# Kernel tuning notes

Hardware: AMD Instinct MI355X
Metric: run time of the kernel (lower is better)

Reference implementation:

```python
import jax, jax.numpy as jnp
from jax import lax
import numpy as np

NF = 64      # feature channels
G = 8        # deformable groups
K = 3        # kernel size
KK = K * K
NLEVEL = 3

PARAM_SHAPES = {
    "c0a_w": (64, 3, 3, 3), "c0a_b": (64,),
    "c0r_w1": (64, 64, 3, 3), "c0r_b1": (64,), "c0r_w2": (64, 64, 3, 3), "c0r_b2": (64,),
    "c0b_w": (64, 64, 3, 3), "c0b_b": (64,),
    "d_r1w1": (64, 64, 3, 3), "d_r1b1": (64,), "d_r1w2": (64, 64, 3, 3), "d_r1b2": (64,),
    "d_r2w1": (64, 64, 3, 3), "d_r2b1": (64,), "d_r2w2": (64, 64, 3, 3), "d_r2b2": (64,),
    "d_cw": (64, 64, 3, 3), "d_cb": (64,),
    "off_c1w": (64, 128, 3, 3), "off_c1b": (64,),
    "off_rw1": (64, 64, 3, 3), "off_rb1": (64,), "off_rw2": (64, 64, 3, 3), "off_rb2": (64,),
    "off_c2w": (64, 64, 3, 3), "off_c2b": (64,),
    "mrg_c1w": (64, 128, 3, 3), "mrg_c1b": (64,),
    "mrg_rw1": (64, 64, 3, 3), "mrg_rb1": (64,), "mrg_rw2": (64, 64, 3, 3), "mrg_rb2": (64,),
    "mrg_c2w": (64, 64, 3, 3), "mrg_c2b": (64,),
    "dcn_om_w": (216, 64, 3, 3), "dcn_om_b": (216,),
    "dcn_w": (64, 64, 3, 3), "dcn_b": (64,),
}


def setup_inputs() -> dict:
    key = jax.random.key(0)
    inp = {"images": jax.random.normal(key, (2, 3, 3, 160, 160), jnp.float32)}
    for i, (name, sh) in enumerate(PARAM_SHAPES.items()):
        if len(sh) == 1:
            inp[name] = jnp.zeros(sh, jnp.float32)
        else:
            inp[name] = jax.random.normal(jax.random.fold_in(key, i + 1), sh, jnp.float32) * 0.05
    return inp


def conv(x, w, b):
    y = lax.conv_general_dilated(x, w, (1, 1), 'SAME',
                                 dimension_numbers=('NCHW', 'OIHW', 'NCHW'))
    return y + b[None, :, None, None]


def lrelu(x):  # nn.LeakyReLU default slope 0.01
    return jnp.where(x >= 0, x, 0.01 * x)


def resblock(x, w1, b1, w2, b2):
    return x + conv(jax.nn.relu(conv(x, w1, b1)), w2, b2)


def maxpool3s2(x):  # MaxPool2d(3, 2, 1)
    return lax.reduce_window(x, -jnp.inf, lax.max, (1, 1, 3, 3), (1, 1, 2, 2),
                             ((0, 0), (0, 0), (1, 1), (1, 1)))


def offnet(x, c1w, c1b, rw1, rb1, rw2, rb2, c2w, c2b):
    # Conv-LReLU, then the SAME residual block applied twice (shared), Conv-LReLU
    x = lrelu(conv(x, c1w, c1b))
    x = resblock(x, rw1, rb1, rw2, rb2)
    x = resblock(x, rw1, rb1, rw2, rb2)
    return lrelu(conv(x, c2w, c2b))


def dcn(x, feat, om_w, om_b, w, b):
    # Modulated deformable conv v2 (extra_offset_mask=True): offsets/mask from feat.
    B, C, H, W = x.shape
    Cg = C // G
    om = conv(feat, om_w, om_b)                       # [B, 3*G*KK, H, W]
    o1, o2, m = jnp.split(om, 3, axis=1)
    dy = o1.reshape(B, G, KK, H, W)
    dx = o2.reshape(B, G, KK, H, W)
    mask = jax.nn.sigmoid(m).reshape(B, G, KK, H, W)
    ky, kx = jnp.meshgrid(jnp.arange(K, dtype=x.dtype) - 1,
                          jnp.arange(K, dtype=x.dtype) - 1, indexing='ij')
    py = dy + jnp.arange(H, dtype=x.dtype)[:, None] + ky.reshape(KK)[:, None, None]
    px = dx + jnp.arange(W, dtype=x.dtype) + kx.reshape(KK)[:, None, None]
    y0 = jnp.floor(py); x0 = jnp.floor(px)
    wy = py - y0; wx = px - x0
    y0i = y0.astype(jnp.int32); x0i = x0.astype(jnp.int32)
    xg = x.reshape(B, G, Cg, H * W)

    def gather(yi, xi, wt):
        valid = (yi >= 0) & (yi < H) & (xi >= 0) & (xi < W)
        idx = jnp.clip(yi, 0, H - 1) * W + jnp.clip(xi, 0, W - 1)      # [B,G,KK,H,W]
        g = jnp.take_along_axis(
            xg, jnp.broadcast_to(idx.reshape(B, G, 1, KK * H * W), (B, G, Cg, KK * H * W)),
            axis=3).reshape(B, G, Cg, KK, H, W)
        return g * (wt * valid)[:, :, None]

    val = (gather(y0i, x0i, (1 - wy) * (1 - wx))
           + gather(y0i, x0i + 1, (1 - wy) * wx)
           + gather(y0i + 1, x0i, wy * (1 - wx))
           + gather(y0i + 1, x0i + 1, wy * wx))
    val = val * mask[:, :, None]                      # [B,G,Cg,KK,H,W]
    wr = w.reshape(w.shape[0], G, Cg, KK)
    return jnp.einsum('bgckhw,ogck->bohw', val, wr) + b[None, :, None, None]


def reference(images, c0a_w, c0a_b, c0r_w1, c0r_b1, c0r_w2, c0r_b2, c0b_w, c0b_b,
              d_r1w1, d_r1b1, d_r1w2, d_r1b2, d_r2w1, d_r2b1, d_r2w2, d_r2b2, d_cw, d_cb,
              off_c1w, off_c1b, off_rw1, off_rb1, off_rw2, off_rb2, off_c2w, off_c2b,
              mrg_c1w, mrg_c1b, mrg_rw1, mrg_rb1, mrg_rw2, mrg_rb2, mrg_c2w, mrg_c2b,
              dcn_om_w, dcn_om_b, dcn_w, dcn_b):
    b, n, c, h, w = images.shape
    x = images.reshape(b * n, c, h, w)
    x = conv(x, c0a_w, c0a_b)
    x = resblock(x, c0r_w1, c0r_b1, c0r_w2, c0r_b2)
    feat = lrelu(conv(x, c0b_w, c0b_b))
    pyrs = [feat]
    for _ in range(NLEVEL - 1):  # downs share one parameter set ([module]*n)
        y = resblock(pyrs[-1], d_r1w1, d_r1b1, d_r1w2, d_r1b2)
        y = resblock(y, d_r2w1, d_r2b1, d_r2w2, d_r2b2)
        y = lrelu(maxpool3s2(conv(y, d_cw, d_cb)))
        pyrs.append(y)
    laps = [p.reshape(b, n, NF, p.shape[-2], p.shape[-1]) for p in pyrs]
    offp = (off_c1w, off_c1b, off_rw1, off_rb1, off_rw2, off_rb2, off_c2w, off_c2b)
    mrgp = (mrg_c1w, mrg_c1b, mrg_rw1, mrg_rb1, mrg_rw2, mrg_rb2, mrg_c2w, mrg_c2b)
    cv = n // 2
    for view in range(n):  # sequential in-place update (center view mutates mid-loop)
        po = offnet(jnp.concatenate([laps[-1][:, cv], laps[-1][:, view]], 1), *offp)
        laps[-1] = laps[-1].at[:, view].set(
            dcn(laps[-1][:, view], po, dcn_om_w, dcn_om_b, dcn_w, dcn_b))
        for level in range(NLEVEL - 2, -1, -1):
            cf = laps[level][:, cv]
            lf = laps[level][:, view]
            off = offnet(jnp.concatenate([cf, lf], 1), *offp)
            B_, C_, H_, W_ = po.shape
            po_up = jax.image.resize(po, (B_, C_, H_ * 2, W_ * 2), 'bilinear')
            off = offnet(jnp.concatenate([off, po_up * 2.0], 1), *mrgp)
            laps[level] = laps[level].at[:, view].set(
                dcn(lf, off, dcn_om_w, dcn_om_b, dcn_w, dcn_b))
            po = off
    return tuple(laps)
```

## Files before the change

kernel.cpp:

```cpp
#include <hip/hip_runtime.h>
#include <math.h>

using short8 = __attribute__((ext_vector_type(8))) short;
using f32x4  = __attribute__((ext_vector_type(4))) float;

struct Tab8 { long o[8]; };

__device__ __forceinline__ unsigned short f2bf(float f) {
    unsigned u = __builtin_bit_cast(unsigned, f);
    unsigned r = u + 0x7FFFu + ((u >> 16) & 1u);
    return (unsigned short)(r >> 16);
}
__device__ __forceinline__ float bf2f(unsigned short h) {
    unsigned u = ((unsigned)h) << 16;
    return __builtin_bit_cast(float, u);
}

struct WDesc { const float* w; int Ci, O, Opad; long off; };
struct WDescs { WDesc d[18]; };

__global__ __launch_bounds__(256) void prep_w_k(WDescs ds, unsigned short* wp)
{
    const WDesc d = ds.d[blockIdx.y];
    const int ncib = (d.Ci + 15) >> 4;
    const int n = ncib * d.Opad * 288;
    const int idx = blockIdx.x * 256 + threadIdx.x;
    if (idx >= n) return;
    const int within = idx % 288;
    const int o = (idx / 288) % d.Opad;
    const int cib = idx / (288 * d.Opad);
    const int t = within >> 5, q = within & 31;
    const int ci = (cib << 4) + (q & 15);
    float v = 0.0f;
    if (o < d.O && ci < d.Ci) v = d.w[((long)o * d.Ci + ci) * 9 + t];
    const unsigned short hi = f2bf(v);
    const unsigned short lo = f2bf(v - bf2f(hi));
    wp[d.off + idx] = (q < 16) ? hi : lo;
}

__global__ __launch_bounds__(256) void prep_dcnw_k(const float* __restrict__ w,
                                                   unsigned short* __restrict__ out)
{
    const int idx = blockIdx.x * 256 + threadIdx.x;
    if (idx >= 36 * 64 * 32) return;
    const int q = idx & 31, o = (idx >> 5) & 63, kb = idx >> 11;
    const float v = w[o * 576 + kb * 16 + (q & 15)];
    const unsigned short hi = f2bf(v);
    out[idx] = (q < 16) ? hi : f2bf(v - bf2f(hi));
}

__global__ __launch_bounds__(256, 2) void conv_mfma_k(
    const float* __restrict__ in1, Tab8 t1, int cin1,
    const float* __restrict__ in2, Tab8 t2, int cin2,
    const unsigned short* __restrict__ wp,
    const float* __restrict__ bias,
    const float* __restrict__ res, Tab8 trr, int hasres,
    float* __restrict__ out, Tab8 to,
    int O, int H, int W, int act)
{
    __shared__ unsigned short in_t[12960];
    __shared__ unsigned short w_t[18944];
    const int tid = threadIdx.x;
    const int b = blockIdx.z;
    const int Opad = gridDim.y << 6;
    const int cobase = blockIdx.y << 6;
    const int tilesX = (W + 15) >> 4;
    const int tx = blockIdx.x % tilesX, ty = blockIdx.x / tilesX;
    const int x0 = tx << 4, y0 = ty << 4;
    const int HW = H * W;
    const int cin_tot = cin1 + cin2;
    const int ncib = (cin_tot + 15) >> 4;
    const int wv = tid >> 6, lane = tid & 63;
    const int lxx = lane & 15, kb = lane >> 4;
    const long o1 = t1.o[b], o2 = t2.o[b];

    f32x4 acc[4][4];
    #pragma unroll
    for (int i = 0; i < 4; ++i)
        #pragma unroll
        for (int j = 0; j < 4; ++j)
            acc[i][j] = (f32x4){0.f, 0.f, 0.f, 0.f};

    for (int cib = 0; cib < ncib; ++cib) {
        __syncthreads();
        const unsigned short* slab = wp + ((long)cib * Opad + cobase) * 288;
        #pragma unroll
        for (int i = 0; i < 9; ++i) {
            const int c = tid + (i << 8);
            const int row = c / 36, col = c - row * 36;
            *(short8*)&w_t[row * 296 + (col << 3)] =
                *(const short8*)(slab + row * 288 + (col << 3));
        }
        if (tid < 144) {
            const int yy = tid >> 3, rp = tid & 7;
            const int g = (cib << 4) + (rp << 1);
            const float* s0 = nullptr;
            const float* s1 = nullptr;
            if (g < cin_tot)
                s0 = (g < cin1) ? in1 + o1 + (long)g * HW
                                : in2 + o2 + (long)(g - cin1) * HW;
            if (g + 1 < cin_tot)
                s1 = (g + 1 < cin1) ? in1 + o1 + (long)(g + 1) * HW
                                    : in2 + o2 + (long)(g + 1 - cin1) * HW;
            const int gy = y0 - 1 + yy;
            const bool yok = (gy >= 0) && (gy < H);
            #pragma unroll
            for (int xx = 0; xx < 18; ++xx) {
                const int gx = x0 - 1 + xx;
                const bool ok = yok && (gx >= 0) && (gx < W);
                const float v0 = (ok && s0) ? s0[gy * W + gx] : 0.0f;
                const float v1 = (ok && s1) ? s1[gy * W + gx] : 0.0f;
                const unsigned short h0 = f2bf(v0), h1 = f2bf(v1);
                const unsigned short l0 = f2bf(v0 - bf2f(h0));
                const unsigned short l1 = f2bf(v1 - bf2f(h1));
                unsigned short* base = &in_t[(yy * 18 + xx) * 40];
                *(unsigned*)(base + (rp << 1))      = (unsigned)h0 | ((unsigned)h1 << 16);
                *(unsigned*)(base + 16 + (rp << 1)) = (unsigned)l0 | ((unsigned)l1 << 16);
            }
        }
        __syncthreads();
        #pragma unroll
        for (int ky = 0; ky < 3; ++ky) {
            #pragma unroll
            for (int kx = 0; kx < 3; ++kx) {
                const int tap = ky * 3 + kx;
                short8 a[4], b1[4], b2[4];
                #pragma unroll
                for (int mt = 0; mt < 4; ++mt)
                    a[mt] = *(const short8*)&w_t[(mt * 16 + lxx) * 296 + tap * 32 + kb * 8];
                #pragma unroll
                for (int rr = 0; rr < 4; ++rr) {
                    const int pbase = ((wv * 4 + rr + ky) * 18 + lxx + kx) * 40;
                    b1[rr] = *(const short8*)&in_t[pbase + kb * 8];
                    b2[rr] = *(const short8*)&in_t[pbase + (kb ^ 2) * 8];
                }
                #pragma unroll
                for (int mt = 0; mt < 4; ++mt)
                    #pragma unroll
                    for (int rr = 0; rr < 4; ++rr) {
                        acc[mt][rr] = __builtin_amdgcn_mfma_f32_16x16x32_bf16(
                            a[mt], b1[rr], acc[mt][rr], 0, 0, 0);
                        acc[mt][rr] = __builtin_amdgcn_mfma_f32_16x16x32_bf16(
                            a[mt], b2[rr], acc[mt][rr], 0, 0, 0);
                    }
            }
        }
    }

    const int x = x0 + lxx;
    const bool xok = (x < W);
    const long ob = to.o[b], rb = trr.o[b];
    #pragma unroll
    for (int mt = 0; mt < 4; ++mt) {
        const int col0 = cobase + mt * 16 + kb * 4;
        float bvv[4];
        #pragma unroll
        for (int j = 0; j < 4; ++j)
            bvv[j] = (col0 + j < O) ? bias[col0 + j] : 0.0f;
        #pragma unroll
        for (int rr = 0; rr < 4; ++rr) {
            const int y = y0 + wv * 4 + rr;
            if (y >= H) continue;
            #pragma unroll
            for (int j = 0; j < 4; ++j) {
                const int coj = col0 + j;
                if (coj >= O || !xok) continue;
                float v = acc[mt][rr][j] + bvv[j];
                if (hasres) v += res[rb + (long)coj * HW + (long)y * W + x];
                if (act == 1) v = fmaxf(v, 0.0f);
                else if (act == 2) v = (v >= 0.0f) ? v : 0.01f * v;
                out[ob + (long)coj * HW + (long)y * W + x] = v;
            }
        }
    }
}

__global__ __launch_bounds__(256) void pool_lrelu_k(
    const float* __restrict__ in, float* __restrict__ out, int H, int W)
{
    const int Ho = H / 2, Wo = W / 2;
    const int n = blockIdx.y;
    const int i = blockIdx.x * 256 + threadIdx.x;
    if (i >= Ho * Wo) return;
    const int ho = i / Wo, wo = i % Wo;
    const float* p = in + (long)n * H * W;
    float m = -1e30f;
    #pragma unroll
    for (int dy = 0; dy < 3; ++dy) {
        const int y = 2 * ho - 1 + dy;
        if (y < 0 || y >= H) continue;
        #pragma unroll
        for (int dx = 0; dx < 3; ++dx) {
            const int x = 2 * wo - 1 + dx;
            if (x < 0 || x >= W) continue;
            m = fmaxf(m, p[y * W + x]);
        }
    }
    out[(long)n * Ho * Wo + i] = (m >= 0.0f) ? m : 0.01f * m;
}

__global__ __launch_bounds__(256) void resize2x_k(
    const float* __restrict__ in, float* __restrict__ out, int H, int W)
{
    const int Ho = 2 * H, Wo = 2 * W;
    const int n = blockIdx.y;
    const int i = blockIdx.x * 256 + threadIdx.x;
    if (i >= Ho * Wo) return;
    const int ho = i / Wo, wo = i % Wo;
    float cy = fminf(fmaxf(0.5f * (ho + 0.5f) - 0.5f, 0.0f), (float)(H - 1));
    float cx = fminf(fmaxf(0.5f * (wo + 0.5f) - 0.5f, 0.0f), (float)(W - 1));
    const int y0 = (int)cy, x0 = (int)cx;
    const int y1 = min(y0 + 1, H - 1), x1 = min(x0 + 1, W - 1);
    const float fy = cy - y0, fx = cx - x0;
    const float* p = in + (long)n * H * W;
    const float v = (1.0f - fy) * ((1.0f - fx) * p[y0 * W + x0] + fx * p[y0 * W + x1])
                  + fy * ((1.0f - fx) * p[y1 * W + x0] + fx * p[y1 * W + x1]);
    out[(long)n * Ho * Wo + i] = 2.0f * v;
}

__global__ __launch_bounds__(256) void nhwc_k(
    const float* __restrict__ src, Tab8 ts, float* __restrict__ dst,
    long dstride, int HW)
{
    __shared__ float t[64][65];
    const int tid = threadIdx.x;
    const int vb = blockIdx.y;
    const int pos0 = blockIdx.x * 64;
    const float* s = src + ts.o[vb];
    float* d = dst + (long)vb * dstride;
    const int l = tid & 63, q = tid >> 6;
    #pragma unroll
    for (int i = 0; i < 16; ++i) {
        const int c = q * 16 + i;
        t[c][l] = s[(long)c * HW + pos0 + l];
    }
    __syncthreads();
    #pragma unroll
    for (int i = 0; i < 16; ++i) {
        const int p = q * 16 + i;
        d[(long)(pos0 + p) * 64 + l] = t[l][p];
    }
}

__global__ __launch_bounds__(256, 2) void dcn_mfma_k(
    const float* __restrict__ xT, long xtstride,
    const float* __restrict__ om, long omstride,
    const unsigned short* __restrict__ wp,
    const float* __restrict__ bias,
    float* __restrict__ outb, Tab8 toff,
    int H, int W)
{
    __shared__ unsigned short valb[9][32][40];
    __shared__ float rw0[576], rw1[576], rw2[576], rw3[576];
    __shared__ int ridx[576], rdd[576];

    const int tid = threadIdx.x;
    const int vb = blockIdx.y;
    const int HW = H * W;
    const int pos0 = blockIdx.x * 32;
    const float* xv = xT + (long)vb * xtstride;
    const float* omv = om + (long)vb * omstride;
    const int lane = tid & 63, wv = tid >> 6;
    const int lxx = lane & 15, kq = lane >> 4;

    f32x4 acc[2];
    acc[0] = (f32x4){0.f, 0.f, 0.f, 0.f};
    acc[1] = (f32x4){0.f, 0.f, 0.f, 0.f};

    for (int gp = 0; gp < 4; ++gp) {
        for (int r = tid; r < 576; r += 256) {
            const int p = r & 31;
            const int gk = r >> 5;
            const int g2 = (gk >= 9) ? 1 : 0;
            const int kk = gk - g2 * 9;
            const int g = gp * 2 + g2;
            const int pos = pos0 + p;
            const int hh = pos / W, ww = pos % W;
            const int ch = g * 9 + kk;
            const float dy = omv[(long)ch * HW + pos];
            const float dx = omv[(long)(72 + ch) * HW + pos];
            const float mv = omv[(long)(144 + ch) * HW + pos];
            const float m = 1.0f / (1.0f + expf(-mv));
            float py = dy + (float)(hh + kk / 3 - 1);
            float px = dx + (float)(ww + kk % 3 - 1);
            py = fminf(fmaxf(py, -8.0f), (float)H + 8.0f);
            px = fminf(fmaxf(px, -8.0f), (float)W + 8.0f);
            const float yf = floorf(py), xf = floorf(px);
            const float wy = py - yf, wx = px - xf;
            const int y0 = (int)yf, x0 = (int)xf;
            const int y1 = y0 + 1, x1 = x0 + 1;
            const bool yv0 = (y0 >= 0) && (y0 < H), yv1 = (y1 >= 0) && (y1 < H);
            const bool xv0_ = (x0 >= 0) && (x0 < W), xv1_ = (x1 >= 0) && (x1 < W);
            const int yc0 = min(max(y0, 0), H - 1), yc1 = min(max(y1, 0), H - 1);
            const int xc0 = min(max(x0, 0), W - 1), xc1 = min(max(x1, 0), W - 1);
            rw0[r] = (yv0 && xv0_) ? (1.f - wy) * (1.f - wx) * m : 0.f;
            rw1[r] = (yv0 && xv1_) ? (1.f - wy) * wx * m : 0.f;
            rw2[r] = (yv1 && xv0_) ? wy * (1.f - wx) * m : 0.f;
            rw3[r] = (yv1 && xv1_) ? wy * wx * m : 0.f;
            ridx[r] = yc0 * W + xc0;
            rdd[r] = (xc1 - xc0) | (((yc1 - yc0) * W) << 8);
        }
        __syncthreads();
        for (int r = tid; r < 576; r += 256) {
            const int p = r & 31;
            const int gk = r >> 5;
            const int g2 = (gk >= 9) ? 1 : 0;
            const int kk = gk - g2 * 9;
            const int g = gp * 2 + g2;
            const float w0 = rw0[r], w1 = rw1[r], w2 = rw2[r], w3 = rw3[r];
            const int dd = rdd[r];
            const long b00 = ((long)ridx[r] << 6) + (g << 3);
            const long d01 = (long)(dd & 0xff) << 6;
            const long d10 = (long)(dd >> 8) << 6;
            const float4 aA = *(const float4*)(xv + b00);
            const float4 aB = *(const float4*)(xv + b00 + 4);
            const float4 bA = *(const float4*)(xv + b00 + d01);
            const float4 bB = *(const float4*)(xv + b00 + d01 + 4);
            const float4 cA = *(const float4*)(xv + b00 + d10);
            const float4 cB = *(const float4*)(xv + b00 + d10 + 4);
            const float4 dA = *(const float4*)(xv + b00 + d10 + d01);
            const float4 dB = *(const float4*)(xv + b00 + d10 + d01 + 4);
            const int kb0 = g * 72 + kk;
#define DO_CH(VAL, C) { \
            const float v_ = (VAL); \
            const int k_ = kb0 + 9 * (C); \
            const int kbl_ = (k_ >> 4) - gp * 9; \
            const int q_ = k_ & 15; \
            const unsigned short hi_ = f2bf(v_); \
            valb[kbl_][p][q_] = hi_; \
            valb[kbl_][p][q_ + 16] = f2bf(v_ - bf2f(hi_)); }
            DO_CH(w0 * aA.x + w1 * bA.x + w2 * cA.x + w3 * dA.x, 0)
            DO_CH(w0 * aA.y + w1 * bA.y + w2 * cA.y + w3 * dA.y, 1)
            DO_CH(w0 * aA.z + w1 * bA.z + w2 * cA.z + w3 * dA.z, 2)
            DO_CH(w0 * aA.w + w1 * bA.w + w2 * cA.w + w3 * dA.w, 3)
            DO_CH(w0 * aB.x + w1 * bB.x + w2 * cB.x + w3 * dB.x, 4)
            DO_CH(w0 * aB.y + w1 * bB.y + w2 * cB.y + w3 * dB.y, 5)
            DO_CH(w0 * aB.z + w1 * bB.z + w2 * cB.z + w3 * dB.z, 6)
            DO_CH(w0 * aB.w + w1 * bB.w + w2 * cB.w + w3 * dB.w, 7)
#undef DO_CH
        }
        __syncthreads();
        #pragma unroll
        for (int kb = 0; kb < 9; ++kb) {
            const short8 a = *(const short8*)(
                wp + ((long)(gp * 9 + kb) * 64 + wv * 16 + lxx) * 32 + kq * 8);
            #pragma unroll
            for (int pt = 0; pt < 2; ++pt) {
                const short8 v1 = *(const short8*)&valb[kb][pt * 16 + lxx][kq * 8];
                const short8 v2 = *(const short8*)&valb[kb][pt * 16 + lxx][(kq ^ 2) * 8];
                acc[pt] = __builtin_amdgcn_mfma_f32_16x16x32_bf16(a, v1, acc[pt], 0, 0, 0);
                acc[pt] = __builtin_amdgcn_mfma_f32_16x16x32_bf16(a, v2, acc[pt], 0, 0, 0);
            }
        }
        __syncthreads();
    }
    float* ov = outb + toff.o[vb];
    #pragma unroll
    for (int pt = 0; pt < 2; ++pt)
        #pragma unroll
        for (int j = 0; j < 4; ++j) {
            const int o = wv * 16 + kq * 4 + j;
            const int p = pt * 16 + lxx;
            ov[(long)o * HW + pos0 + p] = acc[pt][j] + bias[o];
        }
}

namespace {

struct MOff {
    const unsigned short *c1w; const float* c1b;
    const unsigned short *rw1; const float* rb1;
    const unsigned short *rw2; const float* rb2;
    const unsigned short *c2w; const float* c2b;
};

inline Tab8 tab(long stride) {
    Tab8 t;
    for (int i = 0; i < 8; ++i) t.o[i] = (long)i * stride;
    return t;
}

inline void conv_b(hipStream_t s,
                   const float* i1, Tab8 t1, int c1,
                   const float* i2, Tab8 t2, int c2,
                   const unsigned short* w, const float* bias,
                   const float* res, Tab8 trr, int hasres,
                   float* out, Tab8 to,
                   int O, int Opad, int H, int W, int B, int act)
{
    dim3 grid(((H + 15) / 16) * ((W + 15) / 16), Opad / 64, B);
    conv_mfma_k<<<grid, 256, 0, s>>>(i1, t1, c1, i2, t2, c2, w, bias,
                                     res, trr, hasres, out, to, O, H, W, act);
}

inline void offnetB(hipStream_t s, const MOff& p,
                    const float* cfb, Tab8 tcf, const float* lfb, Tab8 tlf,
                    float* t1, float* u, float* outp, int H, int W, int B)
{
    const long hw = (long)H * W;
    const Tab8 tz = tab(64 * hw);
    conv_b(s, cfb, tcf, 64, lfb, tlf, 64, p.c1w, p.c1b,
           nullptr, tz, 0, t1, tz, 64, 64, H, W, B, 2);
    for (int r = 0; r < 2; ++r) {
        conv_b(s, t1, tz, 64, nullptr, tz, 0, p.rw1, p.rb1,
               nullptr, tz, 0, u, tz, 64, 64, H, W, B, 1);
        conv_b(s, u, tz, 64, nullptr, tz, 0, p.rw2, p.rb2,
               t1, tz, 1, t1, tz, 64, 64, H, W, B, 0);
    }
    conv_b(s, t1, tz, 64, nullptr, tz, 0, p.c2w, p.c2b,
           nullptr, tz, 0, outp, tz, 64, 64, H, W, B, 2);
}

inline void dcnB(hipStream_t s, float* lapbase, Tab8 tlf,
                 const float* feat,
                 const unsigned short* Wom, const float* omb,
                 const unsigned short* Wdcn, const float* dcnb,
                 float* om, float* xt, int H, int W, int VB)
{
    const long hw = (long)H * W;
    const long SZf = 64L * 25600;
    int cmax = (int)((8L * SZf) / (216 * hw));
    const int cx = (int)((4L * SZf) / (64 * hw));
    if (cx < cmax) cmax = cx;
    if (cmax > VB) cmax = VB;
    if (cmax < 1) cmax = 1;
    for (int c0 = 0; c0 < VB; c0 += cmax) {
        const int nc = (VB - c0 < cmax) ? (VB - c0) : cmax;
        Tab8 tfeat = tab(0), tx = tab(0);
        for (int i = 0; i < nc; ++i) {
            tfeat.o[i] = (long)(c0 + i) * 64 * hw;
            tx.o[i]    = tlf.o[c0 + i];
        }
        dim3 gt((int)(hw / 64), nc);
        nhwc_k<<<gt, 256, 0, s>>>(lapbase, tx, xt, 64 * hw, (int)hw);
        conv_b(s, feat, tfeat, 64, nullptr, tfeat, 0, Wom, omb,
               nullptr, tfeat, 0, om, tab(216 * hw), 216, 256, H, W, nc, 0);
        dim3 gd((int)(hw / 32), nc);
        dcn_mfma_k<<<gd, 256, 0, s>>>(xt, 64 * hw, om, 216 * hw, Wdcn, dcnb,
                                      lapbase, tx, H, W);
    }
}

}

extern "C" void kernel_launch(void* const* d_in, const int* in_sizes, int n_in,
                              void* d_out, int out_size, void* d_ws, size_t ws_size,
                              hipStream_t stream)
{
    (void)in_sizes; (void)n_in; (void)out_size; (void)ws_size;
    const float* P[39];
    for (int k = 0; k < 39; ++k) P[k] = (const float*)d_in[k];
    const float* images = P[0];

    const int HW0 = 160 * 160, HW1 = 80 * 80, HW2 = 40 * 40;
    float* L0 = (float*)d_out;
    float* L1 = L0 + (long)6 * 64 * HW0;
    float* L2 = L1 + (long)6 * 64 * HW1;

    const long SZ = (long)64 * HW0;
    float* ws = (float*)d_ws;
    float* OFF_A = ws;
    float* OFF_B = ws + 4 * SZ;
    float* POUP  = ws + 8 * SZ;
    float* T1    = ws + 12 * SZ;
    float* U     = POUP;
    float* OM    = ws + 8 * SZ;
    float* A     = ws;
    float* Bb    = ws + 6 * SZ;
    unsigned short* WP = (unsigned short*)(ws + 16 * SZ);

    const int widx[18] = {1,3,5,7,9,11,13,15,17,19,21,23,25,27,29,31,33,35};
    const int wci[18]  = {3,64,64,64,64,64,64,64,64,128,64,64,64,128,64,64,64,64};
    const int wo_[18]  = {64,64,64,64,64,64,64,64,64,64,64,64,64,64,64,64,64,216};
    WDescs ds;
    long off = 0;
    long woff[18];
    for (int i = 0; i < 18; ++i) {
        const int opad = (wo_[i] + 63) / 64 * 64;
        const int ncib = (wci[i] + 15) / 16;
        ds.d[i].w = P[widx[i]]; ds.d[i].Ci = wci[i]; ds.d[i].O = wo_[i];
        ds.d[i].Opad = opad; ds.d[i].off = off;
        woff[i] = off;
        off += (long)ncib * opad * 288;
    }
    unsigned short* WPD = WP + off;
    prep_w_k<<<dim3(1152, 18), 256, 0, stream>>>(ds, WP);
    prep_dcnw_k<<<dim3(288), 256, 0, stream>>>(P[37], WPD);

    const unsigned short* Wc0a  = WP + woff[0];
    const unsigned short* Wc0r1 = WP + woff[1];
    const unsigned short* Wc0r2 = WP + woff[2];
    const unsigned short* Wc0b  = WP + woff[3];
    const unsigned short* Wd11  = WP + woff[4];
    const unsigned short* Wd12  = WP + woff[5];
    const unsigned short* Wd21  = WP + woff[6];
    const unsigned short* Wd22  = WP + woff[7];
    const unsigned short* Wdc   = WP + woff[8];
    MOff offp = {WP + woff[9],  P[20], WP + woff[10], P[22],
                 WP + woff[11], P[24], WP + woff[12], P[26]};
    MOff mrgp = {WP + woff[13], P[28], WP + woff[14], P[30],
                 WP + woff[15], P[32], WP + woff[16], P[34]};
    const unsigned short* Wom = WP + woff[17];
    const float* dcn_om_b = P[36];
    const float* dcn_b = P[38];

    const Tab8 ti = tab((long)3 * HW0);
    const Tab8 t60 = tab((long)64 * HW0);
    const Tab8 t61 = tab((long)64 * HW1);
    conv_b(stream, images, ti, 3, nullptr, t60, 0, Wc0a, P[2],
           nullptr, t60, 0, A, t60, 64, 64, 160, 160, 6, 0);
    conv_b(stream, A, t60, 64, nullptr, t60, 0, Wc0r1, P[4],
           nullptr, t60, 0, Bb, t60, 64, 64, 160, 160, 6, 1);
    conv_b(stream, Bb, t60, 64, nullptr, t60, 0, Wc0r2, P[6],
           A, t60, 1, A, t60, 64, 64, 160, 160, 6, 0);
    conv_b(stream, A, t60, 64, nullptr, t60, 0, Wc0b, P[8],
           nullptr, t60, 0, L0, t60, 64, 64, 160, 160, 6, 2);

    conv_b(stream, L0, t60, 64, nullptr, t60, 0, Wd11, P[10],
           nullptr, t60, 0, Bb, t60, 64, 64, 160, 160, 6, 1);
    conv_b(stream, Bb, t60, 64, nullptr, t60, 0, Wd12, P[12],
           L0, t60, 1, A, t60, 64, 64, 160, 160, 6, 0);
    conv_b(stream, A, t60, 64, nullptr, t60, 0, Wd21, P[14],
           nullptr, t60, 0, Bb, t60, 64, 64, 160, 160, 6, 1);
    conv_b(stream, Bb, t60, 64, nullptr, t60, 0, Wd22, P[16],
           A, t60, 1, A, t60, 64, 64, 160, 160, 6, 0);
    conv_b(stream, A, t60, 64, nullptr, t60, 0, Wdc, P[18],
           nullptr, t60, 0, Bb, t60, 64, 64, 160, 160, 6, 0);
    {
        dim3 gp((HW1 + 255) / 256, 6 * 64);
        pool_lrelu_k<<<gp, 256, 0, stream>>>(Bb, L1, 160, 160);
    }
    conv_b(stream, L1, t61, 64, nullptr, t61, 0, Wd11, P[10],
           nullptr, t61, 0, Bb, t61, 64, 64, 80, 80, 6, 1);
    conv_b(stream, Bb, t61, 64, nullptr, t61, 0, Wd12, P[12],
           L1, t61, 1, A, t61, 64, 64, 80, 80, 6, 0);
    conv_b(stream, A, t61, 64, nullptr, t61, 0, Wd21, P[14],
           nullptr, t61, 0, Bb, t61, 64, 64, 80, 80, 6, 1);
    conv_b(stream, Bb, t61, 64, nullptr, t61, 0, Wd22, P[16],
           A, t61, 1, A, t61, 64, 64, 80, 80, 6, 0);
    conv_b(stream, A, t61, 64, nullptr, t61, 0, Wdc, P[18],
           nullptr, t61, 0, Bb, t61, 64, 64, 80, 80, 6, 0);
    {
        dim3 gp((HW2 + 255) / 256, 6 * 64);
        pool_lrelu_k<<<gp, 256, 0, stream>>>(Bb, L2, 80, 80);
    }

    const int cv = 1;
    for (int pass = 0; pass < 2; ++pass) {
        const int vs01[2] = {0, 1};
        const int vs2[1] = {2};
        const int* vlist = pass ? vs2 : vs01;
        const int nv = pass ? 1 : 2;
        const int VB = nv * 2;

        Tab8 tcf2 = tab(0), tlf2 = tab(0), tcf1 = tab(0), tlf1 = tab(0),
             tcf0 = tab(0), tlf0 = tab(0);
        for (int i = 0; i < VB; ++i) {
            const int v = vlist[i >> 1], b = i & 1;
            tlf2.o[i] = ((long)b * 3 + v)  * 64 * HW2;
            tcf2.o[i] = ((long)b * 3 + cv) * 64 * HW2;
            tlf1.o[i] = ((long)b * 3 + v)  * 64 * HW1;
            tcf1.o[i] = ((long)b * 3 + cv) * 64 * HW1;
            tlf0.o[i] = ((long)b * 3 + v)  * 64 * HW0;
            tcf0.o[i] = ((long)b * 3 + cv) * 64 * HW0;
        }
        offnetB(stream, offp, L2, tcf2, L2, tlf2, T1, U, OFF_A, 40, 40, VB);
        dcnB(stream, L2, tlf2, OFF_A, Wom, dcn_om_b, WPD, dcn_b,
             OM, OFF_B, 40, 40, VB);
        offnetB(stream, offp, L1, tcf1, L1, tlf1, T1, U, OFF_B, 80, 80, VB);
        {
            dim3 gr((HW1 + 255) / 256, VB * 64);
            resize2x_k<<<gr, 256, 0, stream>>>(OFF_A, POUP, 40, 40);
        }
        offnetB(stream, mrgp, OFF_B, tab((long)64 * HW1), POUP, tab((long)64 * HW1),
                T1, U, OFF_A, 80, 80, VB);
        dcnB(stream, L1, tlf1, OFF_A, Wom, dcn_om_b, WPD, dcn_b,
             OM, OFF_B, 80, 80, VB);
        offnetB(stream, offp, L0, tcf0, L0, tlf0, T1, U, OFF_B, 160, 160, VB);
        {
            dim3 gr((HW0 + 255) / 256, VB * 64);
            resize2x_k<<<gr, 256, 0, stream>>>(OFF_A, POUP, 80, 80);
        }
        offnetB(stream, mrgp, OFF_B, tab((long)64 * HW0), POUP, tab((long)64 * HW0),
                T1, U, OFF_A, 160, 160, VB);
        dcnB(stream, L0, tlf0, OFF_A, Wom, dcn_om_b, WPD, dcn_b,
             OM, OFF_B, 160, 160, VB);
    }
}
```

Before: 6.258 ms.

## Prefetch next channel block into registers during MFMA compute in conv kernel

The conv kernel now loads the next input-channel block's weights and input tile from global memory into registers while the current block's MFMA work runs, then writes them to shared memory at the start of the next iteration. This software pipelining is meant to hide global memory latency behind compute. In exchange it holds 9 short8 vectors and 36 floats per thread in registers, which may lower occupancy or cause spills.

```diff
diff --git a/kernel.cpp b/kernel.cpp
--- a/kernel.cpp
+++ b/kernel.cpp
@@ -74,6 +74,40 @@
     const int lxx = lane & 15, kb = lane >> 4;
     const long o1 = t1.o[b], o2 = t2.o[b];
 
+    const bool stager = tid < 144;
+    const int syy = tid >> 3, srp = tid & 7;
+    const int sgy = y0 - 1 + syy;
+    const bool syok = (sgy >= 0) && (sgy < H);
+
+    float h0[18], h1[18];
+    short8 wreg[9];
+
+    {
+        const unsigned short* slab = wp + ((long)0 * Opad + cobase) * 288;
+        #pragma unroll
+        for (int i = 0; i < 9; ++i) {
+            const int c = tid + (i << 8);
+            const int row = c / 36, col = c - row * 36;
+            wreg[i] = *(const short8*)(slab + row * 288 + (col << 3));
+        }
+        if (stager) {
+            const int g = (srp << 1);
+            const float* s0 = (g < cin_tot)
+                ? ((g < cin1) ? in1 + o1 + (long)g * HW
+                              : in2 + o2 + (long)(g - cin1) * HW) : nullptr;
+            const float* s1 = (g + 1 < cin_tot)
+                ? ((g + 1 < cin1) ? in1 + o1 + (long)(g + 1) * HW
+                                  : in2 + o2 + (long)(g + 1 - cin1) * HW) : nullptr;
+            #pragma unroll
+            for (int xx = 0; xx < 18; ++xx) {
+                const int gx = x0 - 1 + xx;
+                const bool ok = syok && (gx >= 0) && (gx < W);
+                h0[xx] = (ok && s0) ? s0[sgy * W + gx] : 0.0f;
+                h1[xx] = (ok && s1) ? s1[sgy * W + gx] : 0.0f;
+            }
+        }
+    }
+
     f32x4 acc[4][4];
     #pragma unroll
     for (int i = 0; i < 4; ++i)
@@ -83,42 +117,50 @@
 
     for (int cib = 0; cib < ncib; ++cib) {
         __syncthreads();
-        const unsigned short* slab = wp + ((long)cib * Opad + cobase) * 288;
         #pragma unroll
         for (int i = 0; i < 9; ++i) {
             const int c = tid + (i << 8);
             const int row = c / 36, col = c - row * 36;
-            *(short8*)&w_t[row * 296 + (col << 3)] =
-                *(const short8*)(slab + row * 288 + (col << 3));
-        }
-        if (tid < 144) {
-            const int yy = tid >> 3, rp = tid & 7;
-            const int g = (cib << 4) + (rp << 1);
-            const float* s0 = nullptr;
-            const float* s1 = nullptr;
-            if (g < cin_tot)
-                s0 = (g < cin1) ? in1 + o1 + (long)g * HW
-                                : in2 + o2 + (long)(g - cin1) * HW;
-            if (g + 1 < cin_tot)
-                s1 = (g + 1 < cin1) ? in1 + o1 + (long)(g + 1) * HW
-                                    : in2 + o2 + (long)(g + 1 - cin1) * HW;
-            const int gy = y0 - 1 + yy;
-            const bool yok = (gy >= 0) && (gy < H);
+            *(short8*)&w_t[row * 296 + (col << 3)] = wreg[i];
+        }
+        if (stager) {
             #pragma unroll
             for (int xx = 0; xx < 18; ++xx) {
-                const int gx = x0 - 1 + xx;
-                const bool ok = yok && (gx >= 0) && (gx < W);
-                const float v0 = (ok && s0) ? s0[gy * W + gx] : 0.0f;
-                const float v1 = (ok && s1) ? s1[gy * W + gx] : 0.0f;
-                const unsigned short h0 = f2bf(v0), h1 = f2bf(v1);
-                const unsigned short l0 = f2bf(v0 - bf2f(h0));
-                const unsigned short l1 = f2bf(v1 - bf2f(h1));
-                unsigned short* base = &in_t[(yy * 18 + xx) * 40];
-                *(unsigned*)(base + (rp << 1))      = (unsigned)h0 | ((unsigned)h1 << 16);
-                *(unsigned*)(base + 16 + (rp << 1)) = (unsigned)l0 | ((unsigned)l1 << 16);
+                const unsigned short H0 = f2bf(h0[xx]), H1 = f2bf(h1[xx]);
+                const unsigned short L0 = f2bf(h0[xx] - bf2f(H0));
+                const unsigned short L1 = f2bf(h1[xx] - bf2f(H1));
+                unsigned short* base = &in_t[(syy * 18 + xx) * 40];
+                *(unsigned*)(base + (srp << 1))      = (unsigned)H0 | ((unsigned)H1 << 16);
+                *(unsigned*)(base + 16 + (srp << 1)) = (unsigned)L0 | ((unsigned)L1 << 16);
             }
         }
         __syncthreads();
+        if (cib + 1 < ncib) {
+            const int nc = cib + 1;
+            const unsigned short* slab = wp + ((long)nc * Opad + cobase) * 288;
+            #pragma unroll
+            for (int i = 0; i < 9; ++i) {
+                const int c = tid + (i << 8);
+                const int row = c / 36, col = c - row * 36;
+                wreg[i] = *(const short8*)(slab + row * 288 + (col << 3));
+            }
+            if (stager) {
+                const int g = (nc << 4) + (srp << 1);
+                const float* s0 = (g < cin_tot)
+                    ? ((g < cin1) ? in1 + o1 + (long)g * HW
+                                  : in2 + o2 + (long)(g - cin1) * HW) : nullptr;
+                const float* s1 = (g + 1 < cin_tot)
+                    ? ((g + 1 < cin1) ? in1 + o1 + (long)(g + 1) * HW
+                                      : in2 + o2 + (long)(g + 1 - cin1) * HW) : nullptr;
+                #pragma unroll
+                for (int xx = 0; xx < 18; ++xx) {
+                    const int gx = x0 - 1 + xx;
+                    const bool ok = syok && (gx >= 0) && (gx < W);
+                    h0[xx] = (ok && s0) ? s0[sgy * W + gx] : 0.0f;
+                    h1[xx] = (ok && s1) ? s1[sgy * W + gx] : 0.0f;
+                }
+            }
+        }
         #pragma unroll
         for (int ky = 0; ky < 3; ++ky) {
             #pragma unroll
```

Result: slower. 8.278 ms (+32.3%).
